# Kernel tuning notes

Hardware: AMD Instinct MI355X
Metric: run time of the kernel (lower is better)

## Reference

```python
import jax, jax.numpy as jnp
import numpy as np

ALPHA = 1.0
BETA = 1.0
N_TDA = 16      # n: points subsampled per diagram
Q = 2.0         # Wasserstein order
NN_SIZE = 5     # knn size (self + 4 neighbors)
RADIUS = 0.07
H = 0.03
EPS = 1e-12
B, N = 8, 4096


def _sqdist(a, b):
    # a: [..., M, 3], b: [..., K, 3] -> [..., M, K] squared Euclidean distances
    aa = jnp.sum(a * a, -1)[..., :, None]
    bb = jnp.sum(b * b, -1)[..., None, :]
    ab = jnp.einsum('...md,...kd->...mk', a, b)
    return aa + bb - 2.0 * ab


def _mst_deaths(pts):
    # H0 persistence of Vietoris-Rips complex: births all 0, finite deaths are
    # the edge weights of the MST of the complete graph (Prim's algorithm).
    n = pts.shape[0]
    d = jnp.sqrt(jnp.maximum(_sqdist(pts, pts), 0.0))  # [n, n]
    in_tree = jnp.zeros((n,), bool).at[0].set(True)
    mind = d[0]  # distance from each node to the current tree

    def step(carry, _):
        in_tree, mind = carry
        m = jnp.where(in_tree, jnp.inf, mind)
        j = jnp.argmin(m)
        w = m[j]
        in_tree = in_tree.at[j].set(True)
        mind = jnp.minimum(mind, d[j])
        return (in_tree, mind), w

    _, deaths = jax.lax.scan(step, (in_tree, mind), None, length=n - 1)
    return deaths  # [n-1]


def _forward(pred, gt, pcd_radius):
    b = pred.shape[0]
    # ---- EMD loss (nearest-neighbor surrogate of CUDA auction_match) ----
    cost = _sqdist(pred, gt)                              # [B, N, N]
    idx = jnp.argmin(cost, axis=-1)                       # [B, N]
    matched = jnp.take_along_axis(gt, idx[..., None], axis=1)
    d2 = jnp.mean(((pred - matched) ** 2).reshape(b, -1), axis=1, keepdims=True)
    emd = jnp.mean(d2 / pcd_radius)
    # ---- Repulsion loss ----
    dpp = _sqdist(pred, pred)                             # [B, N, N]
    _, knn = jax.lax.top_k(-dpp, NN_SIZE)                 # nearest incl. self
    knn = knn[:, :, 1:]                                   # drop self -> [B, N, 4]
    grouped = jax.vmap(lambda p, ix: p[ix])(pred, knn)    # [B, N, 4, 3]
    r2 = jnp.maximum(jnp.sum((grouped - pred[:, :, None, :]) ** 2, -1), EPS)
    dist = jnp.sqrt(r2)
    rep = jnp.mean((RADIUS - dist) * jnp.exp(-r2 / H ** 2))
    # ---- TDA loss (per-sample VR H0 diagram + q-Wasserstein) ----
    key = jax.random.key(42)
    kp, kg = jax.random.split(key)

    def sub(k, pts):
        ix = jax.random.permutation(k, pts.shape[0])[:N_TDA]
        return pts[ix]

    pred_s = jax.vmap(sub)(jax.random.split(kp, b), pred)  # [B, 16, 3]
    gt_s = jax.vmap(sub)(jax.random.split(kg, b), gt)
    dp = jnp.sort(jax.vmap(_mst_deaths)(pred_s), axis=-1)  # [B, 15]
    dg = jnp.sort(jax.vmap(_mst_deaths)(gt_s), axis=-1)
    wd = jnp.sum(jnp.abs(dp - dg) ** Q, axis=-1) ** (1.0 / Q)
    tda = jnp.mean(wd)
    return (emd * 100.0, rep * ALPHA, tda * BETA)


def setup_inputs() -> dict:
    key = jax.random.key(0)
    k1, k2, k3 = jax.random.split(key, 3)
    pred = jax.random.normal(k1, (B, N, 3), jnp.float32)
    gt = jax.random.normal(k2, (B, N, 3), jnp.float32)
    pcd_radius = jax.random.uniform(k3, (B, 1), jnp.float32) + 0.5
    return {"pred": pred, "gt": gt, "pcd_radius": pcd_radius}


def reference(pred, gt, pcd_radius):
    return _forward(pred, gt, pcd_radius)
```

## Files before the change

### kernel.cpp

```cpp
#include <hip/hip_runtime.h>
#include <cstdint>
#include <cmath>
#include <vector>
#include <algorithm>
#include <numeric>

#define B_SZ 8
#define N_PTS 4096
#define TBLK 256
#define NSPLIT 4
#define JTILE (N_PTS / NSPLIT)

struct TdaArgs { int idx[16][16]; };

#define WS_BT(p)   ((float*)(p))
#define WS_KNN(p)  ((int*)((char*)(p) + 0x80000))
#define WS_PART(p) ((double*)((char*)(p) + 0x300000))

__global__ __launch_bounds__(TBLK, 4)
void pair_kernel(const float* __restrict__ pred, const float* __restrict__ gt,
                 float* __restrict__ bt_out, int* __restrict__ knn_out) {
  __shared__ float4 sg[JTILE];

  const int tid   = threadIdx.x;
  const int chunk = blockIdx.x;
  const int b     = blockIdx.y;
  const int q     = blockIdx.z % NSPLIT;
  const int job   = blockIdx.z / NSPLIT;
  const int jbase = q * JTILE;

  const float* src = (job == 0 ? gt : pred) + ((size_t)b * N_PTS + jbase) * 3;
  for (int j = tid; j < JTILE; j += TBLK) {
    float x = src[3 * j + 0];
    float y = src[3 * j + 1];
    float z = src[3 * j + 2];
    sg[j] = make_float4(x, y, z, -0.5f * fmaf(x, x, fmaf(y, y, z * z)));
  }

  const int i = chunk * TBLK + tid;
  const float* pp = pred + ((size_t)b * N_PTS + i) * 3;
  const float px = pp[0], py = pp[1], pz = pp[2];
  __syncthreads();

  if (job == 0) {
    float bt = -INFINITY;
    for (int j0 = 0; j0 < JTILE; j0 += 8) {
      float t[8];
      #pragma unroll
      for (int k = 0; k < 8; ++k) {
        float4 g = sg[j0 + k];
        t[k] = fmaf(px, g.x, fmaf(py, g.y, fmaf(pz, g.z, g.w)));
      }
      #pragma unroll
      for (int k = 0; k < 8; ++k) bt = fmaxf(bt, t[k]);
    }
    bt_out[((size_t)q * B_SZ + b) * N_PTS + i] = bt;
  } else {
    float t0 = -INFINITY, t1 = -INFINITY, t2 = -INFINITY, t3 = -INFINITY, t4 = -INFINITY;
    int   i0 = 0, i1 = 0, i2 = 0, i3 = 0, i4 = 0;
    for (int j0 = 0; j0 < JTILE; j0 += 8) {
      float t[8];
      #pragma unroll
      for (int k = 0; k < 8; ++k) {
        float4 g = sg[j0 + k];
        t[k] = fmaf(px, g.x, fmaf(py, g.y, fmaf(pz, g.z, g.w)));
      }
      float gm = fmaxf(fmaxf(fmaxf(t[0], t[1]), fmaxf(t[2], t[3])),
                       fmaxf(fmaxf(t[4], t[5]), fmaxf(t[6], t[7])));
      if (gm > t4) {
        #pragma unroll
        for (int k = 0; k < 8; ++k) {
          if (t[k] > t4) {
            t4 = t[k]; i4 = j0 + k;
            if (t4 > t3) { float f = t3; t3 = t4; t4 = f; int p_ = i3; i3 = i4; i4 = p_; }
            if (t3 > t2) { float f = t2; t2 = t3; t3 = f; int p_ = i2; i2 = i3; i3 = p_; }
            if (t2 > t1) { float f = t1; t1 = t2; t2 = f; int p_ = i1; i1 = i2; i2 = p_; }
            if (t1 > t0) { float f = t0; t0 = t1; t1 = f; int p_ = i0; i0 = i1; i1 = p_; }
          }
        }
      }
    }
    int* o = knn_out + (((size_t)q * B_SZ + b) * N_PTS + i) * 5;
    o[0] = jbase + i0; o[1] = jbase + i1; o[2] = jbase + i2;
    o[3] = jbase + i3; o[4] = jbase + i4;
  }
}

__global__ __launch_bounds__(TBLK)
void merge_kernel(const float* __restrict__ pred,
                  const float* __restrict__ bt_in, const int* __restrict__ knn_in,
                  double* __restrict__ partials) {
  __shared__ double wred[2][TBLK / 64];
  const int tid = threadIdx.x;
  const int blk = blockIdx.x;
  const int b   = blk >> 4;
  const int i   = (blk & 15) * TBLK + tid;

  const float* pb = pred + (size_t)b * N_PTS * 3;
  const float px = pb[3 * i + 0], py = pb[3 * i + 1], pz = pb[3 * i + 2];
  const float pn = fmaf(px, px, fmaf(py, py, pz * pz));

  float bt = -INFINITY;
  #pragma unroll
  for (int q = 0; q < NSPLIT; ++q)
    bt = fmaxf(bt, bt_in[((size_t)q * B_SZ + b) * N_PTS + i]);
  double emd = (double)fmaf(-2.0f, bt, pn);

  float s0 = INFINITY, s1 = INFINITY, s2 = INFINITY, s3 = INFINITY;
  int   j0v = 0x7fffffff, j1v = 0x7fffffff, j2v = 0x7fffffff, j3v = 0x7fffffff;
  #pragma unroll
  for (int q = 0; q < NSPLIT; ++q) {
    const int* kn = knn_in + (((size_t)q * B_SZ + b) * N_PTS + i) * 5;
    #pragma unroll
    for (int c = 0; c < 5; ++c) {
      int idx = kn[c];
      float gx = pb[3 * idx + 0], gy = pb[3 * idx + 1], gz = pb[3 * idx + 2];
      float dx = px - gx, dy = py - gy, dz = pz - gz;
      float r2 = fmaf(dx, dx, fmaf(dy, dy, dz * dz));
      if (idx == i) r2 = INFINITY;
      bool lt3 = (r2 < s3) || (r2 == s3 && idx < j3v);
      if (lt3) {
        s3 = r2; j3v = idx;
        if ((s3 < s2) || (s3 == s2 && j3v < j2v)) { float f = s2; s2 = s3; s3 = f; int p_ = j2v; j2v = j3v; j3v = p_; }
        if ((s2 < s1) || (s2 == s1 && j2v < j1v)) { float f = s1; s1 = s2; s2 = f; int p_ = j1v; j1v = j2v; j2v = p_; }
        if ((s1 < s0) || (s1 == s0 && j1v < j0v)) { float f = s0; s0 = s1; s1 = f; int p_ = j0v; j0v = j1v; j1v = p_; }
      }
    }
  }
  double rep = 0.0;
  {
    float rr[4] = { s0, s1, s2, s3 };
    #pragma unroll
    for (int k = 0; k < 4; ++k) {
      float r2 = fmaxf(rr[k], 1e-12f);
      float dist = sqrtf(r2);
      rep += (double)((0.07f - dist) * expf(-r2 / 9.0e-4f));
    }
  }

  double v0 = emd, v1 = rep;
  #pragma unroll
  for (int off = 32; off > 0; off >>= 1) { v0 += __shfl_down(v0, off); v1 += __shfl_down(v1, off); }
  if ((tid & 63) == 0) { wred[0][tid >> 6] = v0; wred[1][tid >> 6] = v1; }
  __syncthreads();
  if (tid == 0) {
    double a = 0.0, r = 0.0;
    #pragma unroll
    for (int w = 0; w < TBLK / 64; ++w) { a += wred[0][w]; r += wred[1][w]; }
    partials[blk * 2 + 0] = a;
    partials[blk * 2 + 1] = r;
  }
}

__global__ __launch_bounds__(64)
void final_kernel(const float* __restrict__ pred, const float* __restrict__ gt,
                  const float* __restrict__ pcd, const double* __restrict__ partials,
                  float* __restrict__ out, TdaArgs args) {
  __shared__ float pts[16][16][3];
  __shared__ float aa[16][16];
  __shared__ float mind[16][16];
  __shared__ float deaths[16][15];
  __shared__ float wd[8];
  const int tid = threadIdx.x;

  if (tid < 16) {
    const float* src = (tid < 8) ? (pred + (size_t)tid * N_PTS * 3)
                                 : (gt + (size_t)(tid - 8) * N_PTS * 3);
    for (int k = 0; k < 16; ++k) {
      int ix = args.idx[tid][k];
      float x = src[3 * ix + 0], y = src[3 * ix + 1], z = src[3 * ix + 2];
      pts[tid][k][0] = x; pts[tid][k][1] = y; pts[tid][k][2] = z;
      aa[tid][k] = x * x + y * y + z * z;
    }
    #define DFORM(j, k) \
      sqrtf(fmaxf(aa[tid][j] + aa[tid][k] - 2.0f * (pts[tid][j][0] * pts[tid][k][0] + \
            pts[tid][j][1] * pts[tid][k][1] + pts[tid][j][2] * pts[tid][k][2]), 0.0f))
    for (int k = 0; k < 16; ++k) mind[tid][k] = DFORM(0, k);
    unsigned mask = 1u;
    for (int step = 0; step < 15; ++step) {
      float best = INFINITY; int bj = 0;
      for (int k = 0; k < 16; ++k) {
        float m = ((mask >> k) & 1u) ? INFINITY : mind[tid][k];
        if (m < best) { best = m; bj = k; }
      }
      deaths[tid][step] = best;
      mask |= (1u << bj);
      for (int k = 0; k < 16; ++k) mind[tid][k] = fminf(mind[tid][k], DFORM(bj, k));
    }
    #undef DFORM
    for (int a = 1; a < 15; ++a) {
      float v = deaths[tid][a];
      int c = a;
      while (c > 0 && deaths[tid][c - 1] > v) { deaths[tid][c] = deaths[tid][c - 1]; --c; }
      deaths[tid][c] = v;
    }
  }
  __syncthreads();
  if (tid < 8) {
    float s = 0.0f;
    for (int k = 0; k < 15; ++k) {
      float d = deaths[tid][k] - deaths[tid + 8][k];
      s += d * d;
    }
    wd[tid] = sqrtf(s);
  }
  __syncthreads();
  if (tid == 0) {
    double tda = 0.0;
    for (int b = 0; b < 8; ++b) tda += (double)wd[b];
    tda /= 8.0;
    double emd = 0.0;
    for (int b = 0; b < 8; ++b) {
      double s = 0.0;
      for (int c = 0; c < 16; ++c) s += partials[(b * 16 + c) * 2];
      emd += (s / (double)(N_PTS * 3)) / (double)pcd[b];
    }
    emd = emd / 8.0 * 100.0;
    double rep = 0.0;
    for (int k = 0; k < 128; ++k) rep += partials[k * 2 + 1];
    rep /= (double)(B_SZ * N_PTS * 4);
    out[0] = (float)emd;
    out[1] = (float)rep;
    out[2] = (float)tda;
  }
}

static inline uint32_t rotl32(uint32_t x, int d) { return (x << d) | (x >> (32 - d)); }

static void threefry2x32_host(uint32_t k0, uint32_t k1, uint32_t& x0, uint32_t& x1) {
  const uint32_t ks[3] = { k0, k1, k0 ^ k1 ^ 0x1BD11BDAu };
  static const int rot[2][4] = { {13, 15, 26, 6}, {17, 29, 16, 24} };
  x0 += ks[0]; x1 += ks[1];
  for (int i = 0; i < 5; ++i) {
    const int* r = rot[i & 1];
    for (int j = 0; j < 4; ++j) {
      x0 += x1;
      x1 = rotl32(x1, r[j]);
      x1 ^= x0;
    }
    x0 += ks[(i + 1) % 3];
    x1 += ks[(i + 2) % 3] + (uint32_t)(i + 1);
  }
}

static void jax_split_p(const uint32_t key[2], int n, uint32_t (*out)[2]) {
  for (int j = 0; j < n; ++j) {
    uint32_t a = 0u, b = (uint32_t)j;
    threefry2x32_host(key[0], key[1], a, b);
    out[j][0] = a; out[j][1] = b;
  }
}

static void jax_bits32_p(const uint32_t key[2], int n, uint32_t* bits) {
  for (int i = 0; i < n; ++i) {
    uint32_t a = 0u, b = (uint32_t)i;
    threefry2x32_host(key[0], key[1], a, b);
    bits[i] = a ^ b;
  }
}

static void jax_perm_first16(const uint32_t key_in[2], int n, int* out16) {
  std::vector<int> x((size_t)n);
  std::iota(x.begin(), x.end(), 0);
  uint32_t key[2] = { key_in[0], key_in[1] };
  const int rounds = (int)std::ceil(3.0 * std::log((double)n) / std::log(4294967295.0));
  std::vector<uint32_t> bits((size_t)n);
  std::vector<int> ord((size_t)n), nx((size_t)n);
  for (int r = 0; r < rounds; ++r) {
    uint32_t kr[2][2];
    jax_split_p(key, 2, kr);
    key[0] = kr[0][0]; key[1] = kr[0][1];
    jax_bits32_p(kr[1], n, bits.data());
    std::iota(ord.begin(), ord.end(), 0);
    std::stable_sort(ord.begin(), ord.end(),
                     [&](int A, int Bv) { return bits[A] < bits[Bv]; });
    for (int i = 0; i < n; ++i) nx[i] = x[ord[i]];
    x.swap(nx);
  }
  for (int i = 0; i < 16; ++i) out16[i] = x[i];
}

static void compute_tda_indices(TdaArgs& args) {
  const uint32_t root[2] = { 0u, 42u };
  uint32_t kpg[2][2];
  jax_split_p(root, 2, kpg);
  uint32_t kb[B_SZ][2];
  jax_split_p(kpg[0], B_SZ, kb);
  for (int b = 0; b < B_SZ; ++b) jax_perm_first16(kb[b], N_PTS, args.idx[b]);
  jax_split_p(kpg[1], B_SZ, kb);
  for (int b = 0; b < B_SZ; ++b) jax_perm_first16(kb[b], N_PTS, args.idx[8 + b]);
}


extern "C" void kernel_launch(void* const* d_in, const int* in_sizes, int n_in,
                              void* d_out, int out_size, void* d_ws, size_t ws_size,
                              hipStream_t stream) {
  const float* pred = (const float*)d_in[0];
  const float* gt   = (const float*)d_in[1];
  const float* pcd  = (const float*)d_in[2];
  float* out = (float*)d_out;

  TdaArgs targs;
  compute_tda_indices(targs);

  float*  bt   = WS_BT(d_ws);
  int*    knn  = WS_KNN(d_ws);
  double* part = WS_PART(d_ws);

  pair_kernel<<<dim3(N_PTS / TBLK, B_SZ, 2 * NSPLIT), dim3(TBLK), 0, stream>>>(pred, gt, bt, knn);
  merge_kernel<<<dim3(B_SZ * N_PTS / TBLK), dim3(TBLK), 0, stream>>>(pred, bt, knn, part);
  final_kernel<<<dim3(1), dim3(64), 0, stream>>>(pred, gt, pcd, part, out, targs);
}
```

Baseline: 4.762 ms.

## Register-tile query points, prune kNN by radius cutoff, store 16-bit indices

Each thread now handles four query points, so every shared-memory candidate load is reused across them, and the candidate range is split eight ways instead of four. The kNN insertion threshold starts at a squared-distance cutoff of 0.10, so far candidates never enter the insertion sort. Neighbor indices are stored as 16-bit values with a sentinel for empty slots, halving workspace traffic. The cutoff changes semantics: neighbors beyond it are dropped, which only matters through the exp(-r2/H^2) term, where it is negligible in float. Register pressure rises and grid occupancy drops as a result.

Result: slower. 4.875 ms (+2.4%).

```diff
diff --git a/kernel.cpp b/kernel.cpp
--- a/kernel.cpp
+++ b/kernel.cpp
@@ -8,25 +8,28 @@
 #define B_SZ 8
 #define N_PTS 4096
 #define TBLK 256
-#define NSPLIT 4
+#define NSPLIT 8
 #define JTILE (N_PTS / NSPLIT)
+#define ITILE 4
+#define RCUT2 0.10f
 
 struct TdaArgs { int idx[16][16]; };
 
 #define WS_BT(p)   ((float*)(p))
-#define WS_KNN(p)  ((int*)((char*)(p) + 0x80000))
-#define WS_PART(p) ((double*)((char*)(p) + 0x300000))
-
-__global__ __launch_bounds__(TBLK, 4)
+#define WS_KNN(p)  ((unsigned short*)((char*)(p) + 0x100000))
+#define WS_PART(p) ((double*)((char*)(p) + 0x380000))
+
+__global__ __launch_bounds__(TBLK, 2)
 void pair_kernel(const float* __restrict__ pred, const float* __restrict__ gt,
-                 float* __restrict__ bt_out, int* __restrict__ knn_out) {
+                 float* __restrict__ bt_out, unsigned short* __restrict__ knn_out) {
   __shared__ float4 sg[JTILE];
 
-  const int tid   = threadIdx.x;
-  const int chunk = blockIdx.x;
-  const int b     = blockIdx.y;
-  const int q     = blockIdx.z % NSPLIT;
-  const int job   = blockIdx.z / NSPLIT;
+  const int tid  = threadIdx.x;
+  const int xb   = blockIdx.x;
+  const int b    = blockIdx.y;
+  const int zz   = blockIdx.z;
+  const int job  = zz >> 3;
+  const int q    = zz & 7;
   const int jbase = q * JTILE;
 
   const float* src = (job == 0 ? gt : pred) + ((size_t)b * N_PTS + jbase) * 3;
@@ -37,58 +40,81 @@
     sg[j] = make_float4(x, y, z, -0.5f * fmaf(x, x, fmaf(y, y, z * z)));
   }
 
-  const int i = chunk * TBLK + tid;
-  const float* pp = pred + ((size_t)b * N_PTS + i) * 3;
-  const float px = pp[0], py = pp[1], pz = pp[2];
+  const float* pb = pred + (size_t)b * N_PTS * 3;
+  const int ibase = xb * (TBLK * ITILE) + tid;
+  float px[ITILE], py[ITILE], pz[ITILE];
+  #pragma unroll
+  for (int ii = 0; ii < ITILE; ++ii) {
+    int i = ibase + ii * TBLK;
+    px[ii] = pb[3 * i + 0]; py[ii] = pb[3 * i + 1]; pz[ii] = pb[3 * i + 2];
+  }
   __syncthreads();
 
   if (job == 0) {
-    float bt = -INFINITY;
+    float bt[ITILE];
+    #pragma unroll
+    for (int ii = 0; ii < ITILE; ++ii) bt[ii] = -INFINITY;
     for (int j0 = 0; j0 < JTILE; j0 += 8) {
-      float t[8];
+      float4 g[8];
       #pragma unroll
-      for (int k = 0; k < 8; ++k) {
-        float4 g = sg[j0 + k];
-        t[k] = fmaf(px, g.x, fmaf(py, g.y, fmaf(pz, g.z, g.w)));
-      }
+      for (int k = 0; k < 8; ++k) g[k] = sg[j0 + k];
       #pragma unroll
-      for (int k = 0; k < 8; ++k) bt = fmaxf(bt, t[k]);
-    }
-    bt_out[((size_t)q * B_SZ + b) * N_PTS + i] = bt;
-  } else {
-    float t0 = -INFINITY, t1 = -INFINITY, t2 = -INFINITY, t3 = -INFINITY, t4 = -INFINITY;
-    int   i0 = 0, i1 = 0, i2 = 0, i3 = 0, i4 = 0;
-    for (int j0 = 0; j0 < JTILE; j0 += 8) {
-      float t[8];
-      #pragma unroll
-      for (int k = 0; k < 8; ++k) {
-        float4 g = sg[j0 + k];
-        t[k] = fmaf(px, g.x, fmaf(py, g.y, fmaf(pz, g.z, g.w)));
-      }
-      float gm = fmaxf(fmaxf(fmaxf(t[0], t[1]), fmaxf(t[2], t[3])),
-                       fmaxf(fmaxf(t[4], t[5]), fmaxf(t[6], t[7])));
-      if (gm > t4) {
+      for (int ii = 0; ii < ITILE; ++ii) {
         #pragma unroll
         for (int k = 0; k < 8; ++k) {
-          if (t[k] > t4) {
-            t4 = t[k]; i4 = j0 + k;
-            if (t4 > t3) { float f = t3; t3 = t4; t4 = f; int p_ = i3; i3 = i4; i4 = p_; }
-            if (t3 > t2) { float f = t2; t2 = t3; t3 = f; int p_ = i2; i2 = i3; i3 = p_; }
-            if (t2 > t1) { float f = t1; t1 = t2; t2 = f; int p_ = i1; i1 = i2; i2 = p_; }
-            if (t1 > t0) { float f = t0; t0 = t1; t1 = f; int p_ = i0; i0 = i1; i1 = p_; }
-          }
+          float t = fmaf(px[ii], g[k].x, fmaf(py[ii], g[k].y, fmaf(pz[ii], g[k].z, g[k].w)));
+          bt[ii] = fmaxf(bt[ii], t);
         }
       }
     }
-    int* o = knn_out + (((size_t)q * B_SZ + b) * N_PTS + i) * 5;
-    o[0] = jbase + i0; o[1] = jbase + i1; o[2] = jbase + i2;
-    o[3] = jbase + i3; o[4] = jbase + i4;
+    #pragma unroll
+    for (int ii = 0; ii < ITILE; ++ii)
+      bt_out[((size_t)q * B_SZ + b) * N_PTS + ibase + ii * TBLK] = bt[ii];
+  } else {
+    float t0[ITILE], t1[ITILE], t2[ITILE], t3[ITILE], t4[ITILE];
+    int   i0v[ITILE], i1v[ITILE], i2v[ITILE], i3v[ITILE], i4v[ITILE];
+    #pragma unroll
+    for (int ii = 0; ii < ITILE; ++ii) {
+      float pn = fmaf(px[ii], px[ii], fmaf(py[ii], py[ii], pz[ii] * pz[ii]));
+      float tcut = 0.5f * (pn - RCUT2);
+      t0[ii] = tcut; t1[ii] = tcut; t2[ii] = tcut; t3[ii] = tcut; t4[ii] = tcut;
+      i0v[ii] = 0xFFFF; i1v[ii] = 0xFFFF; i2v[ii] = 0xFFFF; i3v[ii] = 0xFFFF; i4v[ii] = 0xFFFF;
+    }
+    #define INS(ii, tt, jj) { \
+      t4[ii] = tt; i4v[ii] = jj; \
+      if (t4[ii] > t3[ii]) { float f = t3[ii]; t3[ii] = t4[ii]; t4[ii] = f; int p_ = i3v[ii]; i3v[ii] = i4v[ii]; i4v[ii] = p_; } \
+      if (t3[ii] > t2[ii]) { float f = t2[ii]; t2[ii] = t3[ii]; t3[ii] = f; int p_ = i2v[ii]; i2v[ii] = i3v[ii]; i3v[ii] = p_; } \
+      if (t2[ii] > t1[ii]) { float f = t1[ii]; t1[ii] = t2[ii]; t2[ii] = f; int p_ = i1v[ii]; i1v[ii] = i2v[ii]; i2v[ii] = p_; } \
+      if (t1[ii] > t0[ii]) { float f = t0[ii]; t0[ii] = t1[ii]; t1[ii] = f; int p_ = i0v[ii]; i0v[ii] = i1v[ii]; i1v[ii] = p_; } }
+    for (int j0 = 0; j0 < JTILE; j0 += 4) {
+      float4 g[4];
+      #pragma unroll
+      for (int k = 0; k < 4; ++k) g[k] = sg[j0 + k];
+      #pragma unroll
+      for (int ii = 0; ii < ITILE; ++ii) {
+        #pragma unroll
+        for (int k = 0; k < 4; ++k) {
+          float t = fmaf(px[ii], g[k].x, fmaf(py[ii], g[k].y, fmaf(pz[ii], g[k].z, g[k].w)));
+          if (t > t4[ii]) INS(ii, t, j0 + k);
+        }
+      }
+    }
+    #undef INS
+    #pragma unroll
+    for (int ii = 0; ii < ITILE; ++ii) {
+      size_t base = (((size_t)q * B_SZ + b) * N_PTS + ibase + ii * TBLK) * 5;
+      knn_out[base + 0] = (i0v[ii] == 0xFFFF) ? 0xFFFF : (unsigned short)(jbase + i0v[ii]);
+      knn_out[base + 1] = (i1v[ii] == 0xFFFF) ? 0xFFFF : (unsigned short)(jbase + i1v[ii]);
+      knn_out[base + 2] = (i2v[ii] == 0xFFFF) ? 0xFFFF : (unsigned short)(jbase + i2v[ii]);
+      knn_out[base + 3] = (i3v[ii] == 0xFFFF) ? 0xFFFF : (unsigned short)(jbase + i3v[ii]);
+      knn_out[base + 4] = (i4v[ii] == 0xFFFF) ? 0xFFFF : (unsigned short)(jbase + i4v[ii]);
+    }
   }
 }
 
 __global__ __launch_bounds__(TBLK)
 void merge_kernel(const float* __restrict__ pred,
-                  const float* __restrict__ bt_in, const int* __restrict__ knn_in,
+                  const float* __restrict__ bt_in, const unsigned short* __restrict__ knn_in,
                   double* __restrict__ partials) {
   __shared__ double wred[2][TBLK / 64];
   const int tid = threadIdx.x;
@@ -110,14 +136,15 @@
   int   j0v = 0x7fffffff, j1v = 0x7fffffff, j2v = 0x7fffffff, j3v = 0x7fffffff;
   #pragma unroll
   for (int q = 0; q < NSPLIT; ++q) {
-    const int* kn = knn_in + (((size_t)q * B_SZ + b) * N_PTS + i) * 5;
+    const unsigned short* kn = knn_in + (((size_t)q * B_SZ + b) * N_PTS + i) * 5;
     #pragma unroll
     for (int c = 0; c < 5; ++c) {
-      int idx = kn[c];
+      int v = kn[c];
+      int idx = v & 0xFFF;
       float gx = pb[3 * idx + 0], gy = pb[3 * idx + 1], gz = pb[3 * idx + 2];
       float dx = px - gx, dy = py - gy, dz = pz - gz;
       float r2 = fmaf(dx, dx, fmaf(dy, dy, dz * dz));
-      if (idx == i) r2 = INFINITY;
+      if (v >= 0xFFFF || idx == i) r2 = INFINITY;
       bool lt3 = (r2 < s3) || (r2 == s3 && idx < j3v);
       if (lt3) {
         s3 = r2; j3v = idx;
@@ -132,9 +159,11 @@
     float rr[4] = { s0, s1, s2, s3 };
     #pragma unroll
     for (int k = 0; k < 4; ++k) {
-      float r2 = fmaxf(rr[k], 1e-12f);
-      float dist = sqrtf(r2);
-      rep += (double)((0.07f - dist) * expf(-r2 / 9.0e-4f));
+      if (rr[k] < 1e30f) {
+        float r2 = fmaxf(rr[k], 1e-12f);
+        float dist = sqrtf(r2);
+        rep += (double)((0.07f - dist) * expf(-r2 / 9.0e-4f));
+      }
     }
   }
 
@@ -303,11 +332,11 @@
   TdaArgs targs;
   compute_tda_indices(targs);
 
-  float*  bt   = WS_BT(d_ws);
-  int*    knn  = WS_KNN(d_ws);
-  double* part = WS_PART(d_ws);
-
-  pair_kernel<<<dim3(N_PTS / TBLK, B_SZ, 2 * NSPLIT), dim3(TBLK), 0, stream>>>(pred, gt, bt, knn);
+  float*          bt   = WS_BT(d_ws);
+  unsigned short* knn  = WS_KNN(d_ws);
+  double*         part = WS_PART(d_ws);
+
+  pair_kernel<<<dim3(N_PTS / (TBLK * ITILE), B_SZ, 2 * NSPLIT), dim3(TBLK), 0, stream>>>(pred, gt, bt, knn);
   merge_kernel<<<dim3(B_SZ * N_PTS / TBLK), dim3(TBLK), 0, stream>>>(pred, bt, knn, part);
   final_kernel<<<dim3(1), dim3(64), 0, stream>>>(pred, gt, pcd, part, out, targs);
 }
```
